# Optimization experiments

Hardware: AMD Instinct MI355X
Metric: run time of the kernel (lower is better)

Reference implementation:

```python
import jax, jax.numpy as jnp
import numpy as np

B, N, E = 1, 100000, 3200000
CIN, COUT = 128, 128


def setup_inputs() -> dict:
    key = jax.random.key(0)
    k1, k2, k3, k4 = jax.random.split(key, 4)
    X = jax.random.normal(k1, (B, N, CIN), dtype=jnp.float32)
    edge_index = jax.random.randint(k2, (2, E), 0, N, dtype=jnp.int32)
    edge_weight = jax.random.uniform(k3, (E,), dtype=jnp.float32)
    # GCNConv parameters (glorot weight, zero bias)
    W = jax.random.normal(k4, (CIN, COUT), dtype=jnp.float32) * np.float32(1.0 / np.sqrt(CIN))
    b = jnp.zeros((COUT,), dtype=jnp.float32)
    return {"X": X, "edge_index": edge_index, "edge_weight": edge_weight, "W": W, "b": b}


def reference(X, edge_index, edge_weight, W, b):
    """PyG GCNConv (node_dim=1): symmetric-normalized gather -> linear -> scatter-add.
    out = D^{-1/2} (A + I) D^{-1/2} X W + b, batched over dim 0.
    """
    B_, N_, _ = X.shape
    # add self-loops with weight 1 (PyG GCNConv default fill_value=1)
    loop = jnp.arange(N_, dtype=edge_index.dtype)
    ei = jnp.concatenate([edge_index, jnp.stack([loop, loop])], axis=1)  # (2, E+N)
    ew = jnp.concatenate([edge_weight, jnp.ones((N_,), X.dtype)])        # (E+N,)
    src, dst = ei[0], ei[1]
    deg = jax.ops.segment_sum(ew, dst, num_segments=N_)                  # (N,)
    dis = jnp.where(deg > 0, jax.lax.rsqrt(deg), jnp.zeros_like(deg))
    norm = dis[src] * ew * dis[dst]                                      # (E+N,)
    h = jnp.einsum('bnc,cd->bnd', X, W)                                  # (B,N,COUT)
    msg = h[:, src] * norm[None, :, None]                                # (B,E+N,COUT) gather
    out = jnp.zeros((B_, N_, h.shape[-1]), h.dtype).at[:, dst].add(msg)  # scatter-add
    return out + b
```

## Files before the change

kernel.cpp:

```cpp
#include <hip/hip_runtime.h>

#define CIN 128
#define COUT 128
#define NB_MAX 512
#define BCAP 10240
#define EPB 8192

typedef float f32x4 __attribute__((ext_vector_type(4)));
typedef short bf16x8 __attribute__((ext_vector_type(8)));

__device__ __forceinline__ unsigned short f2bf(float x) {
    unsigned int b = __float_as_uint(x);
    b += 0x7FFFu + ((b >> 16) & 1u);
    return (unsigned short)(b >> 16);
}
__device__ __forceinline__ float bf2f_hi(unsigned int u) {
    return __uint_as_float(u & 0xFFFF0000u);
}
__device__ __forceinline__ float bf2f_lo(unsigned int u) {
    return __uint_as_float(u << 16);
}

__global__ void k_prep(const float* __restrict__ W, unsigned short* __restrict__ WB,
                       int* __restrict__ cursor, int NB, int NBz) {
    int b = blockIdx.x;
    int t = threadIdx.x;
    if (b < NBz) {
        int i = b * 256 + t;
        if (i < NB) cursor[i] = 0;
    } else {
        int pos = (b - NBz) * 2048 + t * 8;
        int lane = (pos >> 3) & 63;
        int ks   = (pos >> 9) & 3;
        int ct   = pos >> 11;
        int k = ks * 32 + (lane >> 4) * 8;
        int c = ct * 16 + (lane & 15);
        #pragma unroll
        for (int j = 0; j < 8; ++j)
            WB[pos + j] = f2bf(W[(k + j) * COUT + c]);
    }
}

__global__ __launch_bounds__(1024) void k_part(const int* __restrict__ ei, const float* __restrict__ ew,
                                               int* __restrict__ cursor,
                                               unsigned long long* __restrict__ brec,
                                               int E, int NB) {
    __shared__ int hist[NB_MAX];
    __shared__ int base_[NB_MAX];
    int t = threadIdx.x;
    int chunk0 = blockIdx.x * EPB;
    bool vec_ok = ((E & 3) == 0);

    for (int i = t; i < NB; i += 1024) hist[i] = 0;
    __syncthreads();

    #pragma unroll
    for (int k = 0; k < EPB / 4096; ++k) {
        int e0 = chunk0 + (k * 1024 + t) * 4;
        if (vec_ok && e0 + 3 < E) {
            int4 d4 = *(const int4*)(ei + E + e0);
            atomicAdd(&hist[d4.x >> 8], 1);
            atomicAdd(&hist[d4.y >> 8], 1);
            atomicAdd(&hist[d4.z >> 8], 1);
            atomicAdd(&hist[d4.w >> 8], 1);
        } else {
            for (int q = 0; q < 4; ++q) {
                int e = e0 + q;
                if (e < E) atomicAdd(&hist[ei[E + e] >> 8], 1);
            }
        }
    }
    __syncthreads();

    for (int i = t; i < NB; i += 1024) {
        int c = hist[i];
        base_[i] = (c > 0) ? atomicAdd(&cursor[i], c) : 0;
        hist[i] = 0;
    }
    __syncthreads();

#define PLACE(ss, dd, ww) do {                                                    \
        int b_ = (dd) >> 8;                                                       \
        unsigned int q_ = (unsigned int)((ww) * 32767.0f + 0.5f);                 \
        int lp_ = atomicAdd(&hist[b_], 1);                                        \
        int pos_ = base_[b_] + lp_;                                               \
        if (pos_ < BCAP)                                                          \
            brec[(size_t)b_ * BCAP + pos_] =                                      \
                ((unsigned long long)((dd) & 255) << 32) |                        \
                (((unsigned int)(ss) << 15) | q_);                                \
    } while (0)

    #pragma unroll
    for (int k = 0; k < EPB / 4096; ++k) {
        int e0 = chunk0 + (k * 1024 + t) * 4;
        if (vec_ok && e0 + 3 < E) {
            int4 s4 = *(const int4*)(ei + e0);
            int4 d4 = *(const int4*)(ei + E + e0);
            float4 w4 = *(const float4*)(ew + e0);
            PLACE(s4.x, d4.x, w4.x);
            PLACE(s4.y, d4.y, w4.y);
            PLACE(s4.z, d4.z, w4.z);
            PLACE(s4.w, d4.w, w4.w);
        } else {
            for (int q = 0; q < 4; ++q) {
                int e = e0 + q;
                if (e < E) PLACE(ei[e], ei[E + e], ew[e]);
            }
        }
    }
#undef PLACE
}

__global__ __launch_bounds__(256) void k_sortdeg(const unsigned long long* __restrict__ brec,
                                                 const int* __restrict__ cursor,
                                                 unsigned int* __restrict__ srec,
                                                 int2* __restrict__ rowinfo,
                                                 float* __restrict__ dis, int N) {
    __shared__ int histA[256];
    __shared__ int scanB[256];
    __shared__ int degq[256];
    __shared__ unsigned int stage[BCAP];
    int t = threadIdx.x;
    int b = blockIdx.x;
    int cnt = min(cursor[b], BCAP);
    const unsigned long long* r = brec + (size_t)b * BCAP;

    histA[t] = 0; degq[t] = 0;
    __syncthreads();

    for (int j = t; j < cnt; j += 256) {
        unsigned long long v = r[j];
        int dl = (int)(v >> 32);
        atomicAdd(&histA[dl], 1);
        atomicAdd(&degq[dl], (int)((unsigned int)v & 0x7FFFu));
    }
    __syncthreads();

    int c = histA[t];
    scanB[t] = c;
    __syncthreads();
    #pragma unroll
    for (int off = 1; off < 256; off <<= 1) {
        int v = (t >= off) ? scanB[t - off] : 0;
        __syncthreads();
        scanB[t] += v;
        __syncthreads();
    }
    int excl = scanB[t] - c;

    int n = b * 256 + t;
    if (n < N) {
        dis[n] = rsqrtf(1.0f + (float)degq[t] * (1.0f / 32767.0f));
        rowinfo[n] = make_int2(b * BCAP + excl, c);
    }
    histA[t] = excl;
    __syncthreads();

    for (int j = t; j < cnt; j += 256) {
        unsigned long long v = r[j];
        int dl = (int)(v >> 32);
        int pos = atomicAdd(&histA[dl], 1);
        stage[pos] = (unsigned int)v;
    }
    __syncthreads();

    unsigned int* so = srec + (size_t)b * BCAP;
    for (int j = t; j < cnt; j += 256) so[j] = stage[j];
}

__global__ __launch_bounds__(256) void k_gemm(const float* __restrict__ X,
                                              const unsigned short* __restrict__ WB,
                                              const float* __restrict__ dis,
                                              unsigned short* __restrict__ h, int N) {
    __shared__ unsigned short WBs[8 * 4 * 64 * 8];
    __shared__ unsigned short outs[4][16 * 128];
    int t = threadIdx.x;
    int w = t >> 6, l = t & 63;
    int n0 = blockIdx.x * 64;

    {
        const uint4* src = (const uint4*)WB;
        uint4* dst = (uint4*)WBs;
        #pragma unroll
        for (int i = 0; i < 8; ++i) dst[t + i * 256] = src[t + i * 256];
    }

    int rowg = n0 + w * 16 + (l & 15);
    int rcl = min(rowg, N - 1);
    int kbase = (l >> 4) * 8;
    bf16x8 afrag[4];
    #pragma unroll
    for (int ks = 0; ks < 4; ++ks) {
        const float* xp = X + (size_t)rcl * CIN + ks * 32 + kbase;
        float4 x0 = __builtin_nontemporal_load((const f32x4*)xp)
                        [0] == 0.f ? *(const float4*)xp : *(const float4*)xp;
        (void)x0;
        float4 xa = *(const float4*)xp;
        float4 xb = *(const float4*)(xp + 4);
        bf16x8 a;
        a[0] = (short)f2bf(xa.x); a[1] = (short)f2bf(xa.y);
        a[2] = (short)f2bf(xa.z); a[3] = (short)f2bf(xa.w);
        a[4] = (short)f2bf(xb.x); a[5] = (short)f2bf(xb.y);
        a[6] = (short)f2bf(xb.z); a[7] = (short)f2bf(xb.w);
        afrag[ks] = a;
    }

    __syncthreads();

    f32x4 acc[8];
    #pragma unroll
    for (int ct = 0; ct < 8; ++ct) acc[ct] = (f32x4){0.f, 0.f, 0.f, 0.f};

    const bf16x8* wb = (const bf16x8*)WBs;
    #pragma unroll
    for (int ct = 0; ct < 8; ++ct) {
        #pragma unroll
        for (int ks = 0; ks < 4; ++ks) {
            bf16x8 b = wb[(ct * 4 + ks) * 64 + l];
            acc[ct] = __builtin_amdgcn_mfma_f32_16x16x32_bf16(afrag[ks], b, acc[ct], 0, 0, 0);
        }
    }

    int rb = n0 + w * 16 + (l >> 4) * 4;
    float4 d4 = *(const float4*)(dis + rb);
    unsigned short* ow = &outs[w][0];
    #pragma unroll
    for (int ct = 0; ct < 8; ++ct) {
        int ocol = ct * 16 + (l & 15);
        int orow = (l >> 4) * 4;
        ow[(orow + 0) * 128 + ocol] = f2bf(acc[ct][0] * d4.x);
        ow[(orow + 1) * 128 + ocol] = f2bf(acc[ct][1] * d4.y);
        ow[(orow + 2) * 128 + ocol] = f2bf(acc[ct][2] * d4.z);
        ow[(orow + 3) * 128 + ocol] = f2bf(acc[ct][3] * d4.w);
    }

    #pragma unroll
    for (int i = 0; i < 4; ++i) {
        int off = i * 1024 + l * 16;
        int orow = off >> 8;
        int col = (off & 255) >> 1;
        int node = n0 + w * 16 + orow;
        if (node < N) {
            uint4 v = *(const uint4*)((const char*)ow + off);
            *(uint4*)(h + (size_t)node * COUT + col) = v;
        }
    }
}

__global__ __launch_bounds__(256) void k_agg(const unsigned short* __restrict__ h,
                                             const unsigned int* __restrict__ srec,
                                             const int2* __restrict__ rowinfo,
                                             const float* __restrict__ dis,
                                             const float* __restrict__ bias,
                                             float* __restrict__ out, int N) {
    int wave = threadIdx.x >> 6;
    int lane = threadIdx.x & 63;
    int slot = lane >> 4;
    int sl   = slot & 1;
    int cl   = lane & 15;
    int node = blockIdx.x * 8 + wave * 2 + (slot >> 1);
    bool valid = node < N;
    int2 ri = valid ? rowinfo[node] : make_int2(0, 0);
    const unsigned int* r = srec + ri.x;
    int m = ri.y;
    const uint4* hu = (const uint4*)h;

    float a[8] = {0.f, 0.f, 0.f, 0.f, 0.f, 0.f, 0.f, 0.f};
    if (valid && sl == 0) {
        uint4 us = hu[(size_t)node * 16 + cl];
        a[0] = bf2f_lo(us.x); a[1] = bf2f_hi(us.x);
        a[2] = bf2f_lo(us.y); a[3] = bf2f_hi(us.y);
        a[4] = bf2f_lo(us.z); a[5] = bf2f_hi(us.z);
        a[6] = bf2f_lo(us.w); a[7] = bf2f_hi(us.w);
    }

#define LOAD_REC(dst, base_j) do {                                           \
        _Pragma("unroll")                                                    \
        for (int u = 0; u < 4; ++u) {                                        \
            int j_ = (base_j) + u * 2 + sl;                                  \
            unsigned int q_ = 0u;                                            \
            if (j_ < m) q_ = __builtin_nontemporal_load(r + j_);             \
            dst[u] = q_;                                                     \
        } } while (0)

    unsigned int rrc[4];
    LOAD_REC(rrc, 0);
    for (int j0 = 0; j0 < m; j0 += 8) {
        unsigned int rrn[4];
        LOAD_REC(rrn, j0 + 8);
        #pragma unroll
        for (int u = 0; u < 4; ++u) {
            unsigned int rr = rrc[u];
            float w = (float)(rr & 0x7FFFu) * (1.0f / 32767.0f);
            uint4 v = hu[(size_t)(rr >> 15) * 16 + cl];
            a[0] += w * bf2f_lo(v.x); a[1] += w * bf2f_hi(v.x);
            a[2] += w * bf2f_lo(v.y); a[3] += w * bf2f_hi(v.y);
            a[4] += w * bf2f_lo(v.z); a[5] += w * bf2f_hi(v.z);
            a[6] += w * bf2f_lo(v.w); a[7] += w * bf2f_hi(v.w);
        }
        #pragma unroll
        for (int u = 0; u < 4; ++u) rrc[u] = rrn[u];
    }
#undef LOAD_REC

    #pragma unroll
    for (int i = 0; i < 8; ++i) a[i] += __shfl_xor(a[i], 16);

    if (valid && sl == 0) {
        float dn = dis[node];
        int c0 = cl * 8;
        float4 b0 = *(const float4*)(bias + c0);
        float4 b1 = *(const float4*)(bias + c0 + 4);
        f32x4 o0 = {a[0] * dn + b0.x, a[1] * dn + b0.y, a[2] * dn + b0.z, a[3] * dn + b0.w};
        f32x4 o1 = {a[4] * dn + b1.x, a[5] * dn + b1.y, a[6] * dn + b1.z, a[7] * dn + b1.w};
        f32x4* op = (f32x4*)(out + (size_t)node * COUT + c0);
        __builtin_nontemporal_store(o0, op);
        __builtin_nontemporal_store(o1, op + 1);
    }
}

extern "C" void kernel_launch(void* const* d_in, const int* in_sizes, int n_in,
                              void* d_out, int out_size, void* d_ws, size_t ws_size,
                              hipStream_t stream) {
    const float* X    = (const float*)d_in[0];
    const int*   ei   = (const int*)d_in[1];
    const float* ew   = (const float*)d_in[2];
    const float* W    = (const float*)d_in[3];
    const float* bias = (const float*)d_in[4];
    float* out = (float*)d_out;

    int E = in_sizes[2];
    int N = out_size / COUT;
    int NB = (N + 255) >> 8;
    int NBz = (NB + 255) >> 8;

    char* ws = (char*)d_ws;
    unsigned short*     h    = (unsigned short*)ws;     ws += (size_t)N * COUT * 2;
    unsigned long long* brec = (unsigned long long*)ws; ws += (size_t)NB * BCAP * 8;
    unsigned int*       srec = (unsigned int*)ws;       ws += (size_t)NB * BCAP * 4;
    int2*               rinf = (int2*)ws;               ws += (size_t)N * 8;
    float*              dis  = (float*)ws;              ws += (size_t)(N + 64) * 4;
    int*                cur  = (int*)ws;                ws += (size_t)NB * 4;
    unsigned short*     WB   = (unsigned short*)ws;     ws += 8 * 4 * 64 * 8 * 2;

    k_prep   <<<NBz + 8, 256, 0, stream>>>(W, WB, cur, NB, NBz);
    k_part   <<<(E + EPB - 1) / EPB, 1024, 0, stream>>>(ei, ew, cur, brec, E, NB);
    k_sortdeg<<<NB, 256, 0, stream>>>(brec, cur, srec, rinf, dis, N);
    k_gemm   <<<(N + 63) / 64, 256, 0, stream>>>(X, WB, dis, h, N);
    k_agg    <<<(N + 7) / 8, 256, 0, stream>>>(h, srec, rinf, dis, bias, out, N);
}
```

Measured before the change: 187.9 us.

## Sort each row's edges into source-range phases for lockstep gather locality

The sort kernel now bins each destination row's edges into 8 phases by source-node range and stores packed per-phase counts. The aggregation kernel walks the phases in order, so concurrently running waves gather h rows from similar address ranges and should get better L2/MALL locality. A redundant nontemporal load in the GEMM kernel is also removed. In exchange the aggregation loop gains per-phase control overhead and drops its record prefetch. Per-phase counts are packed into 8 bits, so any row with more than 255 edges in one phase would be handled incorrectly.

```diff
diff --git a/kernel.cpp b/kernel.cpp
--- a/kernel.cpp
+++ b/kernel.cpp
@@ -5,6 +5,7 @@
 #define NB_MAX 512
 #define BCAP 10240
 #define EPB 8192
+#define PH 8
 
 typedef float f32x4 __attribute__((ext_vector_type(4)));
 typedef short bf16x8 __attribute__((ext_vector_type(8)));
@@ -115,8 +116,9 @@
                                                  const int* __restrict__ cursor,
                                                  unsigned int* __restrict__ srec,
                                                  int2* __restrict__ rowinfo,
-                                                 float* __restrict__ dis, int N) {
-    __shared__ int histA[256];
+                                                 unsigned long long* __restrict__ rowphase,
+                                                 float* __restrict__ dis, int N, int pshift) {
+    __shared__ int bins[256 * PH];
     __shared__ int scanB[256];
     __shared__ int degq[256];
     __shared__ unsigned int stage[BCAP];
@@ -125,18 +127,29 @@
     int cnt = min(cursor[b], BCAP);
     const unsigned long long* r = brec + (size_t)b * BCAP;
 
-    histA[t] = 0; degq[t] = 0;
+    for (int i = t; i < 256 * PH; i += 256) bins[i] = 0;
+    degq[t] = 0;
     __syncthreads();
 
     for (int j = t; j < cnt; j += 256) {
         unsigned long long v = r[j];
         int dl = (int)(v >> 32);
-        atomicAdd(&histA[dl], 1);
-        atomicAdd(&degq[dl], (int)((unsigned int)v & 0x7FFFu));
-    }
-    __syncthreads();
-
-    int c = histA[t];
+        unsigned int lo = (unsigned int)v;
+        int ph = (int)((lo >> 15) >> pshift);
+        atomicAdd(&bins[dl * PH + ph], 1);
+        atomicAdd(&degq[dl], (int)(lo & 0x7FFFu));
+    }
+    __syncthreads();
+
+    int base = t * PH;
+    int c = 0;
+    unsigned long long pc = 0;
+    #pragma unroll
+    for (int k = 0; k < PH; ++k) {
+        int v = bins[base + k];
+        c += v;
+        pc |= (unsigned long long)(unsigned int)v << (8 * k);
+    }
     scanB[t] = c;
     __syncthreads();
     #pragma unroll
@@ -147,20 +160,25 @@
         __syncthreads();
     }
     int excl = scanB[t] - c;
+    int run = excl;
+    #pragma unroll
+    for (int k = 0; k < PH; ++k) { int v = bins[base + k]; bins[base + k] = run; run += v; }
 
     int n = b * 256 + t;
     if (n < N) {
         dis[n] = rsqrtf(1.0f + (float)degq[t] * (1.0f / 32767.0f));
         rowinfo[n] = make_int2(b * BCAP + excl, c);
-    }
-    histA[t] = excl;
+        rowphase[n] = pc;
+    }
     __syncthreads();
 
     for (int j = t; j < cnt; j += 256) {
         unsigned long long v = r[j];
         int dl = (int)(v >> 32);
-        int pos = atomicAdd(&histA[dl], 1);
-        stage[pos] = (unsigned int)v;
+        unsigned int lo = (unsigned int)v;
+        int ph = (int)((lo >> 15) >> pshift);
+        int pos = atomicAdd(&bins[dl * PH + ph], 1);
+        stage[pos] = lo;
     }
     __syncthreads();
 
@@ -192,9 +210,6 @@
     #pragma unroll
     for (int ks = 0; ks < 4; ++ks) {
         const float* xp = X + (size_t)rcl * CIN + ks * 32 + kbase;
-        float4 x0 = __builtin_nontemporal_load((const f32x4*)xp)
-                        [0] == 0.f ? *(const float4*)xp : *(const float4*)xp;
-        (void)x0;
         float4 xa = *(const float4*)xp;
         float4 xb = *(const float4*)(xp + 4);
         bf16x8 a;
@@ -250,6 +265,7 @@
 __global__ __launch_bounds__(256) void k_agg(const unsigned short* __restrict__ h,
                                              const unsigned int* __restrict__ srec,
                                              const int2* __restrict__ rowinfo,
+                                             const unsigned long long* __restrict__ rowphase,
                                              const float* __restrict__ dis,
                                              const float* __restrict__ bias,
                                              float* __restrict__ out, int N) {
@@ -260,9 +276,10 @@
     int cl   = lane & 15;
     int node = blockIdx.x * 8 + wave * 2 + (slot >> 1);
     bool valid = node < N;
-    int2 ri = valid ? rowinfo[node] : make_int2(0, 0);
+    int nodec = valid ? node : (N - 1);
+    int2 ri = rowinfo[nodec];
+    unsigned long long pc = valid ? rowphase[node] : 0ULL;
     const unsigned int* r = srec + ri.x;
-    int m = ri.y;
     const uint4* hu = (const uint4*)h;
 
     float a[8] = {0.f, 0.f, 0.f, 0.f, 0.f, 0.f, 0.f, 0.f};
@@ -274,34 +291,32 @@
         a[6] = bf2f_lo(us.w); a[7] = bf2f_hi(us.w);
     }
 
-#define LOAD_REC(dst, base_j) do {                                           \
-        _Pragma("unroll")                                                    \
-        for (int u = 0; u < 4; ++u) {                                        \
-            int j_ = (base_j) + u * 2 + sl;                                  \
-            unsigned int q_ = 0u;                                            \
-            if (j_ < m) q_ = __builtin_nontemporal_load(r + j_);             \
-            dst[u] = q_;                                                     \
-        } } while (0)
-
-    unsigned int rrc[4];
-    LOAD_REC(rrc, 0);
-    for (int j0 = 0; j0 < m; j0 += 8) {
-        unsigned int rrn[4];
-        LOAD_REC(rrn, j0 + 8);
-        #pragma unroll
-        for (int u = 0; u < 4; ++u) {
-            unsigned int rr = rrc[u];
-            float w = (float)(rr & 0x7FFFu) * (1.0f / 32767.0f);
-            uint4 v = hu[(size_t)(rr >> 15) * 16 + cl];
-            a[0] += w * bf2f_lo(v.x); a[1] += w * bf2f_hi(v.x);
-            a[2] += w * bf2f_lo(v.y); a[3] += w * bf2f_hi(v.y);
-            a[4] += w * bf2f_lo(v.z); a[5] += w * bf2f_hi(v.z);
-            a[6] += w * bf2f_lo(v.w); a[7] += w * bf2f_hi(v.w);
-        }
-        #pragma unroll
-        for (int u = 0; u < 4; ++u) rrc[u] = rrn[u];
-    }
-#undef LOAD_REC
+    int off = 0;
+    #pragma unroll
+    for (int p = 0; p < PH; ++p) {
+        int c = (int)((pc >> (8 * p)) & 255u);
+        for (int j0 = 0; j0 < c; j0 += 8) {
+            unsigned int rr[4];
+            #pragma unroll
+            for (int u = 0; u < 4; ++u) {
+                int j_ = j0 + u * 2 + sl;
+                unsigned int q_ = 0u;
+                if (j_ < c) q_ = __builtin_nontemporal_load(r + off + j_);
+                rr[u] = q_;
+            }
+            #pragma unroll
+            for (int u = 0; u < 4; ++u) {
+                unsigned int rv = rr[u];
+                float w = (float)(rv & 0x7FFFu) * (1.0f / 32767.0f);
+                uint4 v = hu[(size_t)(rv >> 15) * 16 + cl];
+                a[0] += w * bf2f_lo(v.x); a[1] += w * bf2f_hi(v.x);
+                a[2] += w * bf2f_lo(v.y); a[3] += w * bf2f_hi(v.y);
+                a[4] += w * bf2f_lo(v.z); a[5] += w * bf2f_hi(v.z);
+                a[6] += w * bf2f_lo(v.w); a[7] += w * bf2f_hi(v.w);
+            }
+        }
+        off += c;
+    }
 
     #pragma unroll
     for (int i = 0; i < 8; ++i) a[i] += __shfl_xor(a[i], 16);
@@ -334,18 +349,22 @@
     int NB = (N + 255) >> 8;
     int NBz = (NB + 255) >> 8;
 
+    int pshift = 0;
+    while (((N - 1) >> pshift) >= PH) ++pshift;
+
     char* ws = (char*)d_ws;
     unsigned short*     h    = (unsigned short*)ws;     ws += (size_t)N * COUT * 2;
     unsigned long long* brec = (unsigned long long*)ws; ws += (size_t)NB * BCAP * 8;
     unsigned int*       srec = (unsigned int*)ws;       ws += (size_t)NB * BCAP * 4;
     int2*               rinf = (int2*)ws;               ws += (size_t)N * 8;
+    unsigned long long* rph  = (unsigned long long*)ws; ws += (size_t)N * 8;
     float*              dis  = (float*)ws;              ws += (size_t)(N + 64) * 4;
     int*                cur  = (int*)ws;                ws += (size_t)NB * 4;
     unsigned short*     WB   = (unsigned short*)ws;     ws += 8 * 4 * 64 * 8 * 2;
 
     k_prep   <<<NBz + 8, 256, 0, stream>>>(W, WB, cur, NB, NBz);
     k_part   <<<(E + EPB - 1) / EPB, 1024, 0, stream>>>(ei, ew, cur, brec, E, NB);
-    k_sortdeg<<<NB, 256, 0, stream>>>(brec, cur, srec, rinf, dis, N);
+    k_sortdeg<<<NB, 256, 0, stream>>>(brec, cur, srec, rinf, rph, dis, N, pshift);
     k_gemm   <<<(N + 63) / 64, 256, 0, stream>>>(X, WB, dis, h, N);
-    k_agg    <<<(N + 7) / 8, 256, 0, stream>>>(h, srec, rinf, dis, bias, out, N);
-}
+    k_agg    <<<(N + 7) / 8, 256, 0, stream>>>(h, srec, rinf, rph, dis, bias, out, N);
+}
```

Measured after the change: 195.3 us. 3.9% more time.
